# Kernel tuning notes

Hardware: AMD Instinct MI355X
Metric: run time of the kernel (lower is better)

The kernel has to match this reference:

```python
import jax, jax.numpy as jnp
import numpy as np

B, T, E, H, A, NH = 128, 128, 1024, 1024, 64, 8
SCALE = 1.0 / float(np.sqrt(A))


def setup_inputs() -> dict:
    key = jax.random.key(0)
    ks = jax.random.split(key, 10)
    g = lambda k, shape: jax.random.normal(k, shape, dtype=jnp.float32) * 0.02
    return {
        "encs": jax.random.normal(ks[0], (B, E), dtype=jnp.float32),
        "W_ih": g(ks[1], (3 * H, 2 * E)),
        "W_hh": g(ks[2], (3 * H, H)),
        "b_ih": jnp.zeros((3 * H,), jnp.float32),
        "b_hh": jnp.zeros((3 * H,), jnp.float32),
        "W_mu": g(ks[3], (H, E)),
        "b_mu": jnp.zeros((E,), jnp.float32),
        "W_sig": g(ks[4], (H, E)),
        "b_sig": jnp.zeros((E,), jnp.float32),
        "W_q": g(ks[5], (E, NH * A)),
        "b_q": jnp.zeros((NH * A,), jnp.float32),
        "W_k": g(ks[6], (E, NH * A)),
        "b_k": jnp.zeros((NH * A,), jnp.float32),
        "W_v": g(ks[7], (E, NH * A)),
        "b_v": jnp.zeros((NH * A,), jnp.float32),
        "W_o": g(ks[8], (NH * A, E)),
        "b_o": jnp.zeros((E,), jnp.float32),
    }


def reference(encs, W_ih, W_hh, b_ih, b_hh, W_mu, b_mu, W_sig, b_sig,
              W_q, b_q, W_k, b_k, W_v, b_v, W_o, b_o):
    noise_key = jax.random.key(1234)

    def gru(x, h):  # torch.nn.GRUCell math
        gi = x @ W_ih.T + b_ih
        gh = h @ W_hh.T + b_hh
        ir, iz, inn = jnp.split(gi, 3, axis=-1)
        hr, hz, hn = jnp.split(gh, 3, axis=-1)
        r = jax.nn.sigmoid(ir + hr)
        z = jax.nn.sigmoid(iz + hz)
        n = jnp.tanh(inn + r * hn)
        return (1.0 - z) * n + z * h

    def attn_last(s, i):
        # multi_attn(s,s,s)[:, i]: only row i of softmax is needed (rows independent)
        q = (s[:, :, :] @ W_q + b_q)  # (B,T,NH*A)
        q_i = jax.lax.dynamic_index_in_dim(q, i, axis=1, keepdims=False).reshape(B, NH, A)
        k = (s @ W_k + b_k).reshape(B, T, NH, A)
        v = (s @ W_v + b_v).reshape(B, T, NH, A)
        scores = jnp.einsum("bha,bjha->bhj", q_i, k) * SCALE  # (B,NH,T)
        valid = jnp.arange(T) <= i
        scores = jnp.where(valid[None, None, :], scores, -1e30)
        w = jax.nn.softmax(scores, axis=-1)
        ctx = jnp.einsum("bhj,bjha->bha", w, v).reshape(B, NH * A)
        return ctx @ W_o + b_o  # (B,E)

    def step(carry, i):
        h, mus, sigs, context = carry
        x = jnp.concatenate([encs, context], axis=-1)  # (B,2E)
        h = gru(x, h)
        mu = h @ W_mu + b_mu
        sig = jax.nn.softplus(h @ W_sig + b_sig)
        mus = mus.at[:, i].set(mu)
        sigs = sigs.at[:, i].set(sig)
        eps = jax.random.normal(jax.random.fold_in(noise_key, i), (B, T, E), dtype=jnp.float32)
        valid = (jnp.arange(T) <= i)[None, :, None]
        s = jnp.where(valid, mus + eps * sigs, 0.0)
        context = attn_last(s, i)
        return (h, mus, sigs, context), None

    init = (jnp.zeros((B, H), jnp.float32),
            jnp.zeros((B, T, E), jnp.float32),
            jnp.zeros((B, T, E), jnp.float32),
            jnp.zeros((B, E), jnp.float32))
    (h, mus, sigs, _), _ = jax.lax.scan(step, init, jnp.arange(T))
    # final return is s sampled at step T-1 (all positions valid)
    eps_last = jax.random.normal(jax.random.fold_in(noise_key, T - 1), (B, T, E), dtype=jnp.float32)
    return mus + eps_last * sigs
```

## Files before the change

kernel.cpp:

```cpp
#include <hip/hip_runtime.h>

#define B_   128
#define T_   128
#define E_   1024
#define H_   1024
#define A_   64
#define NH_  8
#define G_   3072
#define QK_  512
#define SCALE_ 0.125f

__device__ __forceinline__ unsigned rotl32(unsigned x, int r) {
  return (x << r) | (x >> (32 - r));
}

__device__ __forceinline__ void tf2x32(unsigned k0, unsigned k1,
                                       unsigned x0, unsigned x1,
                                       unsigned& o0, unsigned& o1) {
  unsigned k2 = k0 ^ k1 ^ 0x1BD11BDAu;
  x0 += k0; x1 += k1;
  x0 += x1; x1 = rotl32(x1, 13); x1 ^= x0;
  x0 += x1; x1 = rotl32(x1, 15); x1 ^= x0;
  x0 += x1; x1 = rotl32(x1, 26); x1 ^= x0;
  x0 += x1; x1 = rotl32(x1,  6); x1 ^= x0;
  x0 += k1; x1 += k2 + 1u;
  x0 += x1; x1 = rotl32(x1, 17); x1 ^= x0;
  x0 += x1; x1 = rotl32(x1, 29); x1 ^= x0;
  x0 += x1; x1 = rotl32(x1, 16); x1 ^= x0;
  x0 += x1; x1 = rotl32(x1, 24); x1 ^= x0;
  x0 += k2; x1 += k0 + 2u;
  x0 += x1; x1 = rotl32(x1, 13); x1 ^= x0;
  x0 += x1; x1 = rotl32(x1, 15); x1 ^= x0;
  x0 += x1; x1 = rotl32(x1, 26); x1 ^= x0;
  x0 += x1; x1 = rotl32(x1,  6); x1 ^= x0;
  x0 += k0; x1 += k1 + 3u;
  x0 += x1; x1 = rotl32(x1, 17); x1 ^= x0;
  x0 += x1; x1 = rotl32(x1, 29); x1 ^= x0;
  x0 += x1; x1 = rotl32(x1, 16); x1 ^= x0;
  x0 += x1; x1 = rotl32(x1, 24); x1 ^= x0;
  x0 += k1; x1 += k2 + 4u;
  x0 += x1; x1 = rotl32(x1, 13); x1 ^= x0;
  x0 += x1; x1 = rotl32(x1, 15); x1 ^= x0;
  x0 += x1; x1 = rotl32(x1, 26); x1 ^= x0;
  x0 += x1; x1 = rotl32(x1,  6); x1 ^= x0;
  x0 += k2; x1 += k0 + 5u;
  o0 = x0; o1 = x1;
}

__device__ __forceinline__ float bits_to_normal(unsigned bits) {
  float uf = __uint_as_float((bits >> 9) | 0x3F800000u) - 1.0f;
  const float LO = -0.99999994f;
  float u = fmaxf(LO, uf * 2.0f + LO);
  float w = -log1pf(-u * u);
  float p;
  if (w < 5.0f) {
    w -= 2.5f;
    p = 2.81022636e-08f;
    p = fmaf(p, w, 3.43273939e-07f);
    p = fmaf(p, w, -3.5233877e-06f);
    p = fmaf(p, w, -4.39150654e-06f);
    p = fmaf(p, w, 0.00021858087f);
    p = fmaf(p, w, -0.00125372503f);
    p = fmaf(p, w, -0.00417768164f);
    p = fmaf(p, w, 0.246640727f);
    p = fmaf(p, w, 1.50140941f);
  } else {
    w = sqrtf(w) - 3.0f;
    p = -0.000200214257f;
    p = fmaf(p, w, 0.000100950558f);
    p = fmaf(p, w, 0.00134934322f);
    p = fmaf(p, w, -0.00367342844f);
    p = fmaf(p, w, 0.00573950773f);
    p = fmaf(p, w, -0.0076224613f);
    p = fmaf(p, w, 0.00943887047f);
    p = fmaf(p, w, 1.00167406f);
    p = fmaf(p, w, 2.83297682f);
  }
  return 1.41421356f * p * u;
}

__device__ __forceinline__ float sigmoidf_(float x) {
  return 1.0f / (1.0f + expf(-x));
}

__device__ __forceinline__ float ld_elem(const void* p, long i, int isb) {
  if (isb) {
    unsigned short u = ((const unsigned short*)p)[i];
    return __uint_as_float(((unsigned)u) << 16);
  }
  return ((const float*)p)[i];
}

__global__ __launch_bounds__(256) void sniff_kernel(const void* encs, int* flag) {
  __shared__ int cnt;
  if (threadIdx.x == 0) cnt = 0;
  __syncthreads();
  const unsigned* w = (const unsigned*)encs;
  int c = 0;
  for (int i = threadIdx.x; i < 4096; i += 256) {
    unsigned e7 = (w[i] >> 8) & 0x7F;
    if (e7 >= 0x3B && e7 <= 0x41) c++;
  }
  atomicAdd(&cnt, c);
  __syncthreads();
  if (threadIdx.x == 0) flag[0] = (cnt > 2048) ? 1 : 0;
}

__global__ __launch_bounds__(256) void conv_kernel(const void* src, float* dst,
                                                   long n, const int* flag) {
  long i = (long)blockIdx.x * 256 + threadIdx.x;
  int isb = flag[0];
  if (i < n) dst[i] = ld_elem(src, i, isb);
}

__global__ __launch_bounds__(256) void trans_kernel(
    const void* W_ih, const void* W_hh, const void* W_mu, const void* W_sig,
    const void* W_k, const float* __restrict__ bihF, const float* __restrict__ bhhF,
    float* __restrict__ Wbig, float* __restrict__ Wms, float* __restrict__ WkT,
    float* __restrict__ Wenc4, float* __restrict__ bias4,
    float* __restrict__ xh, float* __restrict__ h, unsigned* __restrict__ skeys,
    const int* flag)
{
  long idx = (long)blockIdx.x * 256 + threadIdx.x;
  int y = blockIdx.y;
  int isb = flag[0];
  if (y == 0) {
    if (idx < 4194304) {
      int e = (int)(idx & 1023); int col = (int)(idx >> 10);
      int j = col >> 2, c = col & 3;
      float v = 0.f;
      if (c < 3) v = ld_elem(W_ih, (long)(c * 1024 + j) * 2048 + 1024 + e, isb);
      Wbig[(long)e * 4096 + col] = v;
    }
  } else if (y == 1) {
    if (idx < 4194304) {
      int e = (int)(idx & 1023); int col = (int)(idx >> 10);
      int j = col >> 2, c = col & 3;
      float v = 0.f;
      if (c == 0)      v = ld_elem(W_hh, (long)j * 1024 + e, isb);
      else if (c == 1) v = ld_elem(W_hh, (long)(1024 + j) * 1024 + e, isb);
      else if (c == 3) v = ld_elem(W_hh, (long)(2048 + j) * 1024 + e, isb);
      Wbig[(long)(1024 + e) * 4096 + col] = v;
    }
  } else if (y == 2) {
    if (idx < 2097152) {
      int k = (int)(idx >> 11), n = (int)(idx & 2047);
      float v = (n < 1024) ? ld_elem(W_mu, (long)k * 1024 + n, isb)
                           : ld_elem(W_sig, (long)k * 1024 + (n - 1024), isb);
      Wms[idx] = v;
    }
  } else if (y == 3) {
    if (idx < 524288) {
      int qk = (int)(idx >> 10), e = (int)(idx & 1023);
      WkT[idx] = ld_elem(W_k, (long)e * 512 + qk, isb);
    }
    if (idx < 4096) {
      int j = (int)(idx >> 2), c = (int)(idx & 3);
      float v;
      if (c == 0)      v = bihF[j] + bhhF[j];
      else if (c == 1) v = bihF[1024 + j] + bhhF[1024 + j];
      else if (c == 2) v = bihF[2048 + j];
      else             v = bhhF[2048 + j];
      bias4[idx] = v;
    }
    if (idx < 262144) xh[idx] = 0.f;
    if (idx < 131072) h[idx] = 0.f;
    if (idx < 128) {
      unsigned o0, o1;
      tf2x32(0u, 1234u, 0u, (unsigned)idx, o0, o1);
      skeys[2 * idx] = o0; skeys[2 * idx + 1] = o1;
    }
  } else {
    if (idx < 4194304) {
      int e = (int)(idx & 1023); int col = (int)(idx >> 10);
      int j = col >> 2, c = col & 3;
      float v = 0.f;
      if (c < 3) v = ld_elem(W_ih, (long)(c * 1024 + j) * 2048 + e, isb);
      Wenc4[(long)e * 4096 + col] = v;
    }
  }
}

__global__ __launch_bounds__(256) void consts_kernel(
    const float* __restrict__ bqF, const float* __restrict__ bkF,
    const float* __restrict__ bvF, const float* __restrict__ boF,
    const float* __restrict__ WkT, const float* __restrict__ WoF,
    float* __restrict__ bqk, float* __restrict__ qbc, float* __restrict__ bvo)
{
  int idx = blockIdx.x * 256 + threadIdx.x;
  int hh = idx >> 10, e = idx & 1023;
  float s = 0.f;
  for (int a = 0; a < 64; ++a)
    s += bqF[hh * 64 + a] * WkT[(long)(hh * 64 + a) * 1024 + e];
  bqk[idx] = s;
  if (idx < 1024) {
    float v = boF[idx];
    for (int ha = 0; ha < 512; ++ha) v += bvF[ha] * WoF[(long)ha * 1024 + idx];
    bvo[idx] = v;
  }
  if (idx < 8) {
    float v = 0.f;
    for (int a = 0; a < 64; ++a) v += bqF[idx * 64 + a] * bkF[idx * 64 + a];
    qbc[idx] = v;
  }
}

__global__ __launch_bounds__(256) void mm128(
    const float* __restrict__ A, long lda, long zA, int nsumA, long psA,
    const float* __restrict__ Bm, long ldb, long zB,
    float* __restrict__ C, long ldc, long zC, long pstride,
    int Ktot, int S)
{
  int zz = blockIdx.z;
  int head = zz / S, sp = zz - head * S;
  int Kc = Ktot / S;
  long kb = (long)sp * Kc;
  A += (long)head * zA;
  Bm += (long)head * zB;
  C += (long)head * zC + (long)sp * pstride;
  long m0 = (long)blockIdx.y * 128;
  long n0 = (long)blockIdx.x * 128;
  __shared__ float As[16][132];
  __shared__ float Bs[16][132];
  int tid = threadIdx.x;
  int tx = tid & 15, ty = tid >> 4;
  int am = tid >> 2, ac = tid & 3;
  int bk = tid >> 5, bn = tid & 31;
  float acc[8][8];
  #pragma unroll
  for (int i = 0; i < 8; ++i)
    #pragma unroll
    for (int j = 0; j < 8; ++j) acc[i][j] = 0.f;

  for (int k0 = 0; k0 < Kc; k0 += 16) {
    const float* Ap0 = A + (m0 + am) * lda + kb + k0 + 4 * ac;
    const float* Ap1 = A + (m0 + am + 64) * lda + kb + k0 + 4 * ac;
    float4 a0 = *(const float4*)Ap0;
    float4 a1 = *(const float4*)Ap1;
    for (int s2 = 1; s2 < nsumA; ++s2) {
      float4 t0 = *(const float4*)(Ap0 + (long)s2 * psA);
      float4 t1 = *(const float4*)(Ap1 + (long)s2 * psA);
      a0.x += t0.x; a0.y += t0.y; a0.z += t0.z; a0.w += t0.w;
      a1.x += t1.x; a1.y += t1.y; a1.z += t1.z; a1.w += t1.w;
    }
    float4 b0 = *(const float4*)(Bm + (kb + k0 + bk) * ldb + n0 + 4 * bn);
    float4 b1 = *(const float4*)(Bm + (kb + k0 + bk + 8) * ldb + n0 + 4 * bn);
    __syncthreads();
    As[4 * ac + 0][am] = a0.x; As[4 * ac + 1][am] = a0.y;
    As[4 * ac + 2][am] = a0.z; As[4 * ac + 3][am] = a0.w;
    As[4 * ac + 0][am + 64] = a1.x; As[4 * ac + 1][am + 64] = a1.y;
    As[4 * ac + 2][am + 64] = a1.z; As[4 * ac + 3][am + 64] = a1.w;
    *(float4*)&Bs[bk][4 * bn] = b0;
    *(float4*)&Bs[bk + 8][4 * bn] = b1;
    __syncthreads();
    #pragma unroll
    for (int kk = 0; kk < 16; ++kk) {
      float4 av0 = *(const float4*)&As[kk][ty * 4];
      float4 av1 = *(const float4*)&As[kk][64 + ty * 4];
      float4 bv0 = *(const float4*)&Bs[kk][tx * 4];
      float4 bv1 = *(const float4*)&Bs[kk][64 + tx * 4];
      float amv[8] = {av0.x, av0.y, av0.z, av0.w, av1.x, av1.y, av1.z, av1.w};
      float bnv[8] = {bv0.x, bv0.y, bv0.z, bv0.w, bv1.x, bv1.y, bv1.z, bv1.w};
      #pragma unroll
      for (int i = 0; i < 8; ++i)
        #pragma unroll
        for (int j = 0; j < 8; ++j)
          acc[i][j] = fmaf(amv[i], bnv[j], acc[i][j]);
    }
  }

  #pragma unroll
  for (int i = 0; i < 8; ++i) {
    long r = m0 + (long)(i >> 2) * 64 + ty * 4 + (i & 3);
    float4 v0 = {acc[i][0], acc[i][1], acc[i][2], acc[i][3]};
    float4 v1 = {acc[i][4], acc[i][5], acc[i][6], acc[i][7]};
    *(float4*)(C + r * ldc + n0 + tx * 4) = v0;
    *(float4*)(C + r * ldc + n0 + 64 + tx * 4) = v1;
  }
}

__global__ __launch_bounds__(256) void mm64s(
    const float* __restrict__ A, long lda, long zA,
    const float* __restrict__ Bm, long ldb, long zB,
    float* __restrict__ C, long ldc, long zC, long pstride,
    int Ktot, int S)
{
  int zz = blockIdx.z;
  int head = zz / S, sp = zz - head * S;
  int Kc = Ktot / S;
  long kb = (long)sp * Kc;
  A += (long)head * zA; Bm += (long)head * zB;
  C += (long)head * zC + (long)sp * pstride;
  long n0 = (long)blockIdx.x * 64;
  long m0 = (long)blockIdx.y * 64;
  __shared__ float As[16][68];
  __shared__ float Bs[16][68];
  int tid = threadIdx.x;
  int tx = tid & 15, ty = tid >> 4;
  int ar = tid >> 2, ac = tid & 3;
  int br = tid >> 4, bc = tid & 15;
  float acc[4][4];
  #pragma unroll
  for (int i = 0; i < 4; ++i)
    #pragma unroll
    for (int j = 0; j < 4; ++j) acc[i][j] = 0.f;

  for (int k0 = 0; k0 < Kc; k0 += 16) {
    float4 a4 = *(const float4*)(A + (m0 + ar) * lda + kb + k0 + 4 * ac);
    float4 b4 = *(const float4*)(Bm + (kb + k0 + br) * ldb + n0 + 4 * bc);
    __syncthreads();
    As[4 * ac + 0][ar] = a4.x; As[4 * ac + 1][ar] = a4.y;
    As[4 * ac + 2][ar] = a4.z; As[4 * ac + 3][ar] = a4.w;
    *(float4*)(&Bs[br][4 * bc]) = b4;
    __syncthreads();
    #pragma unroll
    for (int kk = 0; kk < 16; ++kk) {
      float4 av = *(const float4*)(&As[kk][4 * ty]);
      float4 bv = *(const float4*)(&Bs[kk][4 * tx]);
      float amv[4] = {av.x, av.y, av.z, av.w};
      float bnv[4] = {bv.x, bv.y, bv.z, bv.w};
      #pragma unroll
      for (int im = 0; im < 4; ++im)
        #pragma unroll
        for (int jn = 0; jn < 4; ++jn)
          acc[im][jn] = fmaf(amv[im], bnv[jn], acc[im][jn]);
    }
  }
  #pragma unroll
  for (int im = 0; im < 4; ++im) {
    long m = m0 + ty * 4 + im;
    float4 v = {acc[im][0], acc[im][1], acc[im][2], acc[im][3]};
    *(float4*)(C + m * ldc + n0 + tx * 4) = v;
  }
}

__global__ __launch_bounds__(256) void gru_epi(
    const float* __restrict__ gsumP, const float* __restrict__ gie4,
    const float* __restrict__ bias4, float* __restrict__ h,
    float* __restrict__ xh)
{
  int idx = blockIdx.x * 256 + threadIdx.x;
  int b = idx >> 10, j = idx & 1023;
  float4 v = ((const float4*)gie4)[(long)b * 1024 + j];
  float4 bb = ((const float4*)bias4)[j];
  v.x += bb.x; v.y += bb.y; v.z += bb.z; v.w += bb.w;
  #pragma unroll
  for (int s = 0; s < 8; ++s) {
    float4 t = ((const float4*)gsumP)[(long)s * 131072 + (long)b * 1024 + j];
    v.x += t.x; v.y += t.y; v.z += t.z; v.w += t.w;
  }
  float r = sigmoidf_(v.x);
  float z = sigmoidf_(v.y);
  float n = tanhf(v.z + r * v.w);
  float ho = h[idx];
  float hn = (1.0f - z) * n + z * ho;
  h[idx] = hn;
  xh[(long)b * 2048 + 1024 + j] = hn;
}

__global__ __launch_bounds__(256) void musig_epi(
    const float* __restrict__ msP, const float* __restrict__ bmuF,
    const float* __restrict__ bsigF, float* __restrict__ mus,
    float* __restrict__ sigs, int step)
{
  int idx = blockIdx.x * 256 + threadIdx.x;
  int b = idx >> 11, n = idx & 2047;
  float v = 0.f;
  #pragma unroll
  for (int s = 0; s < 8; ++s) v += msP[(long)s * 262144 + idx];
  if (n < 1024) {
    mus[((long)b * T_ + step) * E_ + n] = v + bmuF[n];
  } else {
    float x = v + bsigF[n - 1024];
    sigs[((long)b * T_ + step) * E_ + (n - 1024)] =
        fmaxf(x, 0.0f) + log1pf(expf(-fabsf(x)));
  }
}

__global__ __launch_bounds__(256) void gen_s(
    const float* __restrict__ mus, const float* __restrict__ sigs,
    float* __restrict__ s, const unsigned* __restrict__ skeys, int step)
{
  int t = blockIdx.x;
  int b = blockIdx.y;
  int e = threadIdx.x * 4;
  unsigned sk0 = skeys[2 * step], sk1 = skeys[2 * step + 1];
  unsigned f = (unsigned)(b * (T_ * E_) + t * E_ + e);
  unsigned o0, o1;
  float nv[4];
  tf2x32(sk0, sk1, 0u, f + 0u, o0, o1); nv[0] = bits_to_normal(o0 ^ o1);
  tf2x32(sk0, sk1, 0u, f + 1u, o0, o1); nv[1] = bits_to_normal(o0 ^ o1);
  tf2x32(sk0, sk1, 0u, f + 2u, o0, o1); nv[2] = bits_to_normal(o0 ^ o1);
  tf2x32(sk0, sk1, 0u, f + 3u, o0, o1); nv[3] = bits_to_normal(o0 ^ o1);
  long i4 = (((long)b * T_ + t) * E_ + e) >> 2;
  float4 mu = ((const float4*)mus)[i4];
  float4 sg = ((const float4*)sigs)[i4];
  float4 out;
  out.x = fmaf(nv[0], sg.x, mu.x);
  out.y = fmaf(nv[1], sg.y, mu.y);
  out.z = fmaf(nv[2], sg.z, mu.z);
  out.w = fmaf(nv[3], sg.w, mu.w);
  ((float4*)s)[i4] = out;
}

__global__ __launch_bounds__(256) void t_kernel(
    const float* __restrict__ qP, const float* __restrict__ WkT,
    const float* __restrict__ bkF, const float* __restrict__ bqk,
    const float* __restrict__ qbc, float* __restrict__ tmat,
    float* __restrict__ qb)
{
  int e = blockIdx.x * 256 + threadIdx.x;
  int hh = blockIdx.y;
  int b0 = blockIdx.z * 8;
  __shared__ float q_l[8][64];
  int tid = threadIdx.x;
  for (int idx2 = tid; idx2 < 512; idx2 += 256) {
    int bb = idx2 >> 6, a = idx2 & 63;
    float v = 0.f;
    #pragma unroll
    for (int s = 0; s < 8; ++s)
      v += qP[(long)s * 65536 + (long)(b0 + bb) * 512 + hh * 64 + a];
    q_l[bb][a] = v;
  }
  __syncthreads();
  float acc[8];
  #pragma unroll
  for (int bb = 0; bb < 8; ++bb) acc[bb] = 0.f;
  for (int a = 0; a < 64; ++a) {
    float wv = WkT[(long)(hh * 64 + a) * 1024 + e];
    #pragma unroll
    for (int bb = 0; bb < 8; ++bb) acc[bb] = fmaf(q_l[bb][a], wv, acc[bb]);
  }
  float bq_ = bqk[hh * 1024 + e];
  #pragma unroll
  for (int bb = 0; bb < 8; ++bb)
    tmat[((long)(b0 + bb) * NH_ + hh) * 1024 + e] = acc[bb] + bq_;
  if (blockIdx.x == 0 && tid < 8) {
    int bb = tid;
    float sm = qbc[hh];
    for (int a = 0; a < 64; ++a) sm += q_l[bb][a] * bkF[hh * 64 + a];
    qb[(b0 + bb) * NH_ + hh] = sm;
  }
}

__global__ __launch_bounds__(256) void scores_kernel(
    const float* __restrict__ s, const float* __restrict__ tmat,
    const float* __restrict__ qb, float* __restrict__ scg, int step)
{
  int b = blockIdx.y;
  int jbase = blockIdx.x * 32;
  __shared__ float s_ch[32][132];
  __shared__ float t_ch[8][132];
  int tid = threadIdx.x;
  int hh = tid >> 5, jj = tid & 31;
  int j = jbase + jj;
  float acc = 0.f;
  for (int e0 = 0; e0 < 1024; e0 += 128) {
    __syncthreads();
    #pragma unroll
    for (int q = 0; q < 4; ++q) {
      int f = tid + q * 256;
      int jr = f >> 5, e4 = f & 31;
      int jg = jbase + jr;
      if (jg <= step)
        *(float4*)&s_ch[jr][e4 * 4] =
            *(const float4*)&s[((long)b * T_ + jg) * E_ + e0 + e4 * 4];
    }
    {
      int e4 = tid & 31, h2 = tid >> 5;
      *(float4*)&t_ch[h2][e4 * 4] =
          *(const float4*)&tmat[((long)b * NH_ + h2) * E_ + e0 + e4 * 4];
    }
    __syncthreads();
    if (j <= step) {
      #pragma unroll
      for (int e4 = 0; e4 < 32; ++e4) {
        float4 sv = *(const float4*)&s_ch[jj][e4 * 4];
        float4 tv = *(const float4*)&t_ch[hh][e4 * 4];
        acc = fmaf(sv.x, tv.x, acc);
        acc = fmaf(sv.y, tv.y, acc);
        acc = fmaf(sv.z, tv.z, acc);
        acc = fmaf(sv.w, tv.w, acc);
      }
    }
  }
  if (j <= step)
    scg[((long)b * NH_ + hh) * T_ + j] = (acc + qb[b * NH_ + hh]) * SCALE_;
}

__global__ __launch_bounds__(256) void ctx_kernel(
    const float* __restrict__ s, const float* __restrict__ scg,
    float* __restrict__ ctxE, int step)
{
  int b = blockIdx.y;
  int et = blockIdx.x;
  __shared__ float w_l[NH_][T_];
  __shared__ float s_l[32][68];
  int tid = threadIdx.x;
  {
    int hh = tid >> 5, l = tid & 31;
    const float* sc = scg + ((long)b * NH_ + hh) * T_;
    float m = -3.0e38f;
    for (int j = l; j <= step; j += 32) m = fmaxf(m, sc[j]);
    for (int off = 16; off; off >>= 1) m = fmaxf(m, __shfl_xor(m, off, 32));
    float d = 0.f;
    for (int j = l; j <= step; j += 32) {
      float pe = expf(sc[j] - m);
      w_l[hh][j] = pe;
      d += pe;
    }
    for (int off = 16; off; off >>= 1) d += __shfl_xor(d, off, 32);
    float inv = 1.0f / d;
    for (int j = l; j <= step; j += 32) w_l[hh][j] *= inv;
  }
  int e = tid & 63, hp = tid >> 6;
  float acc0 = 0.f, acc1 = 0.f;
  for (int jc = 0; jc <= step; jc += 32) {
    __syncthreads();
    #pragma unroll
    for (int q = 0; q < 8; ++q) {
      int f = tid + q * 256;
      int jr = f >> 6, ee = f & 63;
      int jg = jc + jr;
      if (jg <= step)
        s_l[jr][ee] = s[((long)b * T_ + jg) * E_ + et * 64 + ee];
    }
    __syncthreads();
    int jmax = min(31, step - jc);
    for (int jr = 0; jr <= jmax; ++jr) {
      float sv = s_l[jr][e];
      acc0 = fmaf(w_l[hp][jc + jr], sv, acc0);
      acc1 = fmaf(w_l[hp + 4][jc + jr], sv, acc1);
    }
  }
  ctxE[((long)b * NH_ + hp) * E_ + et * 64 + e] = acc0;
  ctxE[((long)b * NH_ + hp + 4) * E_ + et * 64 + e] = acc1;
}

__global__ __launch_bounds__(256) void fin_kernel(
    const float* __restrict__ ctxvP, const float* __restrict__ bvo,
    float* __restrict__ xh)
{
  int i4 = blockIdx.x * 256 + threadIdx.x;
  int b = i4 >> 8, e4 = i4 & 255;
  float4 v = ((const float4*)bvo)[e4];
  #pragma unroll
  for (int s = 0; s < 4; ++s) {
    float4 t = ((const float4*)ctxvP)[(long)s * 32768 + (long)b * 256 + e4];
    v.x += t.x; v.y += t.y; v.z += t.z; v.w += t.w;
  }
  ((float4*)xh)[(long)b * 512 + e4] = v;
}

extern "C" void kernel_launch(void* const* d_in, const int* in_sizes, int n_in,
                              void* d_out, int out_size, void* d_ws, size_t ws_size,
                              hipStream_t stream) {
  (void)in_sizes; (void)n_in; (void)out_size; (void)ws_size;
  const void* encs  = d_in[0];
  const void* W_ih  = d_in[1];
  const void* W_hh  = d_in[2];
  const void* b_ih  = d_in[3];
  const void* b_hh  = d_in[4];
  const void* W_mu  = d_in[5];
  const void* b_mu  = d_in[6];
  const void* W_sig = d_in[7];
  const void* b_sig = d_in[8];
  const void* W_q   = d_in[9];
  const void* b_q   = d_in[10];
  const void* W_k   = d_in[11];
  const void* b_k   = d_in[12];
  const void* W_v   = d_in[13];
  const void* b_v   = d_in[14];
  const void* W_o   = d_in[15];
  const void* b_o   = d_in[16];

  float* s = (float*)d_out;
  float* w = (float*)d_ws;

  int*   flag   = (int*)w;
  float* p      = w + 1024;
  float* WbigF  = p;  p += (size_t)2048 * 4096;
  float* WmsF   = p;  p += (size_t)1024 * 2048;
  float* WkTF   = p;  p += (size_t)512 * 1024;
  float* WqF    = p;  p += (size_t)1024 * 512;
  float* WvF    = p;  p += (size_t)1024 * 512;
  float* WoF    = p;  p += (size_t)512 * 1024;
  float* encsF  = p;  p += (size_t)B_ * E_;
  float* bihF   = p;  p += 4096;
  float* bhhF   = p;  p += 4096;
  float* bmuF   = p;  p += 1024;
  float* bsigF  = p;  p += 1024;
  float* bqF    = p;  p += 1024;
  float* bkF    = p;  p += 1024;
  float* bvF    = p;  p += 1024;
  float* boF    = p;  p += 1024;
  float* bias4  = p;  p += 4096;
  float* bqk    = p;  p += 8192;
  float* qbc    = p;  p += 1024;
  float* bvo    = p;  p += 1024;
  unsigned* skeys = (unsigned*)p; p += 1024;
  float* gie4   = p;  p += (size_t)B_ * 4096;
  float* xh     = p;  p += (size_t)B_ * 2048;
  float* hbuf   = p;  p += (size_t)B_ * 1024;
  float* gsumP  = p;  p += (size_t)8 * B_ * 4096;
  float* musigP = p;  p += (size_t)8 * B_ * 2048;
  float* qP     = p;  p += (size_t)8 * B_ * 512;
  float* tmat   = p;  p += (size_t)B_ * NH_ * E_;
  float* qbv    = p;  p += 1024;
  float* scg    = p;  p += (size_t)B_ * NH_ * T_;
  float* ctxE   = p;  p += (size_t)B_ * NH_ * E_;
  float* ctxhP  = p;  p += (size_t)4 * B_ * 512;
  float* ctxvP  = p;  p += (size_t)4 * B_ * 1024;
  float* mus    = p;  p += (size_t)B_ * T_ * E_;
  float* sigs   = p;  p += (size_t)B_ * T_ * E_;
  float* Wenc4  = gsumP;

  sniff_kernel<<<1, 256, 0, stream>>>(encs, flag);
  auto conv = [&](const void* src, float* dst, long n) {
    conv_kernel<<<dim3((unsigned)((n + 255) / 256)), 256, 0, stream>>>(src, dst, n, flag);
  };
  conv(encs,  encsF, (long)B_ * E_);
  conv(b_ih,  bihF,  G_);
  conv(b_hh,  bhhF,  G_);
  conv(b_mu,  bmuF,  1024);
  conv(b_sig, bsigF, 1024);
  conv(b_q,   bqF,   512);
  conv(b_k,   bkF,   512);
  conv(b_v,   bvF,   512);
  conv(b_o,   boF,   1024);
  conv(W_q,   WqF,   (long)1024 * 512);
  conv(W_v,   WvF,   (long)1024 * 512);
  conv(W_o,   WoF,   (long)512 * 1024);

  trans_kernel<<<dim3(16384, 5), 256, 0, stream>>>(
      W_ih, W_hh, W_mu, W_sig, W_k, bihF, bhhF,
      WbigF, WmsF, WkTF, Wenc4, bias4, xh, hbuf, skeys, flag);
  consts_kernel<<<dim3(32), 256, 0, stream>>>(
      bqF, bkF, bvF, boF, WkTF, WoF, bqk, qbc, bvo);
  mm128<<<dim3(32, 1, 1), 256, 0, stream>>>(
      encsF, 1024, 0, 1, 0, Wenc4, 4096, 0, gie4, 4096, 0, 0, 1024, 1);

  for (int i = 0; i < T_; ++i) {
    mm128<<<dim3(32, 1, 8), 256, 0, stream>>>(
        xh, 2048, 0, 1, 0, WbigF, 4096, 0, gsumP, 4096, 0, 524288, 2048, 8);
    gru_epi<<<dim3(512), 256, 0, stream>>>(gsumP, gie4, bias4, hbuf, xh);
    mm128<<<dim3(16, 1, 8), 256, 0, stream>>>(
        hbuf, 1024, 0, 1, 0, WmsF, 2048, 0, musigP, 2048, 0, 262144, 1024, 8);
    musig_epi<<<dim3(1024), 256, 0, stream>>>(musigP, bmuF, bsigF, mus, sigs, i);
    gen_s<<<dim3(i + 1, B_), 256, 0, stream>>>(mus, sigs, s, skeys, i);
    mm128<<<dim3(4, 1, 8), 256, 0, stream>>>(
        s + (long)i * E_, (long)T_ * E_, 0, 1, 0, WqF, 512, 0,
        qP, 512, 0, 65536, 1024, 8);
    t_kernel<<<dim3(4, 8, 16), 256, 0, stream>>>(
        qP, WkTF, bkF, bqk, qbc, tmat, qbv);
    scores_kernel<<<dim3((i + 32) / 32, B_), 256, 0, stream>>>(
        s, tmat, qbv, scg, i);
    ctx_kernel<<<dim3(16, B_), 256, 0, stream>>>(s, scg, ctxE, i);
    mm64s<<<dim3(1, 2, 32), 256, 0, stream>>>(
        ctxE, 8192, 1024, WvF, 512, 64, ctxhP, 512, 64, 65536, 1024, 4);
    mm128<<<dim3(8, 1, 4), 256, 0, stream>>>(
        ctxhP, 512, 0, 4, 65536, WoF, 1024, 0, ctxvP, 1024, 0, 131072, 512, 4);
    fin_kernel<<<dim3(128), 256, 0, stream>>>(ctxvP, bvo, xh);
  }
}
```

Measured before the change: 27.35 ms.

## Fuse per-step kernel sequence into persistent megakernel with grid barriers

Replaces the 12 kernel launches per time step (about 1500 in total) with one persistent 256-block megakernel. Stages are separated by a software grid barrier built on atomics. The regeneration of earlier s rows is spread over idle blocks and overlapped with the GEMM stages, and the mu/sigma epilogue is fused with sampling of the current row. This removes launch overhead and tail gaps between small kernels. The cost is many grid-wide barriers per step and a co-residency requirement for all 256 blocks, which risks deadlock if they are not all resident.

```diff
diff --git a/kernel.cpp b/kernel.cpp
--- a/kernel.cpp
+++ b/kernel.cpp
@@ -91,9 +91,36 @@
   return ((const float*)p)[i];
 }
 
+#define NBLK_ 256
+
+__device__ __forceinline__ void gsync(unsigned* bar, int tid) {
+  __syncthreads();
+  if (tid == 0) {
+    __threadfence();
+    unsigned g = __hip_atomic_load(&bar[1], __ATOMIC_RELAXED,
+                                   __HIP_MEMORY_SCOPE_AGENT);
+    unsigned a = __hip_atomic_fetch_add(&bar[0], 1u, __ATOMIC_ACQ_REL,
+                                        __HIP_MEMORY_SCOPE_AGENT);
+    if (a == NBLK_ - 1u) {
+      __hip_atomic_store(&bar[0], 0u, __ATOMIC_RELAXED,
+                         __HIP_MEMORY_SCOPE_AGENT);
+      __hip_atomic_store(&bar[1], g + 1u, __ATOMIC_RELEASE,
+                         __HIP_MEMORY_SCOPE_AGENT);
+    } else {
+      while (__hip_atomic_load(&bar[1], __ATOMIC_RELAXED,
+                               __HIP_MEMORY_SCOPE_AGENT) == g) {
+        __builtin_amdgcn_s_sleep(1);
+      }
+      __threadfence();
+    }
+  }
+  __syncthreads();
+}
+
 __global__ __launch_bounds__(256) void sniff_kernel(const void* encs, int* flag) {
   __shared__ int cnt;
   if (threadIdx.x == 0) cnt = 0;
+  if (threadIdx.x < 2) ((unsigned*)flag)[8 + threadIdx.x] = 0u;
   __syncthreads();
   const unsigned* w = (const unsigned*)encs;
   int c = 0;
@@ -205,24 +232,32 @@
   }
 }
 
-__global__ __launch_bounds__(256) void mm128(
-    const float* __restrict__ A, long lda, long zA, int nsumA, long psA,
-    const float* __restrict__ Bm, long ldb, long zB,
-    float* __restrict__ C, long ldc, long zC, long pstride,
-    int Ktot, int S)
+struct MegaArgs {
+  const float *WbigF, *WmsF, *WkTF, *WqF, *WvF, *WoF;
+  const float *bmuF, *bsigF, *bkF, *bias4, *bqk, *qbc, *bvo;
+  const unsigned *skeys;
+  const float *gie4;
+  float *xh, *hbuf, *gsumP, *musigP, *qP, *tmat, *qbv, *scg;
+  float *ctxE, *ctxhP, *ctxvP, *mus, *sigs, *s;
+  unsigned *bar;
+};
+
+__device__ void mm128_dev(float* smem,
+    const float* A, long lda, long zA, int nsumA, long psA,
+    const float* Bm, long ldb, long zB,
+    float* C, long ldc, long zC, long pstride,
+    int Ktot, int S, int bx, int by, int zz, int tid)
 {
-  int zz = blockIdx.z;
   int head = zz / S, sp = zz - head * S;
   int Kc = Ktot / S;
   long kb = (long)sp * Kc;
   A += (long)head * zA;
   Bm += (long)head * zB;
   C += (long)head * zC + (long)sp * pstride;
-  long m0 = (long)blockIdx.y * 128;
-  long n0 = (long)blockIdx.x * 128;
-  __shared__ float As[16][132];
-  __shared__ float Bs[16][132];
-  int tid = threadIdx.x;
+  long m0 = (long)by * 128;
+  long n0 = (long)bx * 128;
+  float* As = smem;
+  float* Bs = smem + 2112;
   int tx = tid & 15, ty = tid >> 4;
   int am = tid >> 2, ac = tid & 3;
   int bk = tid >> 5, bn = tid & 31;
@@ -246,19 +281,19 @@
     float4 b0 = *(const float4*)(Bm + (kb + k0 + bk) * ldb + n0 + 4 * bn);
     float4 b1 = *(const float4*)(Bm + (kb + k0 + bk + 8) * ldb + n0 + 4 * bn);
     __syncthreads();
-    As[4 * ac + 0][am] = a0.x; As[4 * ac + 1][am] = a0.y;
-    As[4 * ac + 2][am] = a0.z; As[4 * ac + 3][am] = a0.w;
-    As[4 * ac + 0][am + 64] = a1.x; As[4 * ac + 1][am + 64] = a1.y;
-    As[4 * ac + 2][am + 64] = a1.z; As[4 * ac + 3][am + 64] = a1.w;
-    *(float4*)&Bs[bk][4 * bn] = b0;
-    *(float4*)&Bs[bk + 8][4 * bn] = b1;
+    As[(4 * ac + 0) * 132 + am] = a0.x; As[(4 * ac + 1) * 132 + am] = a0.y;
+    As[(4 * ac + 2) * 132 + am] = a0.z; As[(4 * ac + 3) * 132 + am] = a0.w;
+    As[(4 * ac + 0) * 132 + am + 64] = a1.x; As[(4 * ac + 1) * 132 + am + 64] = a1.y;
+    As[(4 * ac + 2) * 132 + am + 64] = a1.z; As[(4 * ac + 3) * 132 + am + 64] = a1.w;
+    *(float4*)&Bs[bk * 132 + 4 * bn] = b0;
+    *(float4*)&Bs[(bk + 8) * 132 + 4 * bn] = b1;
     __syncthreads();
     #pragma unroll
     for (int kk = 0; kk < 16; ++kk) {
-      float4 av0 = *(const float4*)&As[kk][ty * 4];
-      float4 av1 = *(const float4*)&As[kk][64 + ty * 4];
-      float4 bv0 = *(const float4*)&Bs[kk][tx * 4];
-      float4 bv1 = *(const float4*)&Bs[kk][64 + tx * 4];
+      float4 av0 = *(const float4*)&As[kk * 132 + ty * 4];
+      float4 av1 = *(const float4*)&As[kk * 132 + 64 + ty * 4];
+      float4 bv0 = *(const float4*)&Bs[kk * 132 + tx * 4];
+      float4 bv1 = *(const float4*)&Bs[kk * 132 + 64 + tx * 4];
       float amv[8] = {av0.x, av0.y, av0.z, av0.w, av1.x, av1.y, av1.z, av1.w};
       float bnv[8] = {bv0.x, bv0.y, bv0.z, bv0.w, bv1.x, bv1.y, bv1.z, bv1.w};
       #pragma unroll
@@ -279,23 +314,21 @@
   }
 }
 
-__global__ __launch_bounds__(256) void mm64s(
-    const float* __restrict__ A, long lda, long zA,
-    const float* __restrict__ Bm, long ldb, long zB,
-    float* __restrict__ C, long ldc, long zC, long pstride,
-    int Ktot, int S)
+__device__ void mm64s_dev(float* smem,
+    const float* A, long lda, long zA, int nsumA, long psA,
+    const float* Bm, long ldb, long zB,
+    float* C, long ldc, long zC, long pstride,
+    int Ktot, int S, int bx, int by, int zz, int tid)
 {
-  int zz = blockIdx.z;
   int head = zz / S, sp = zz - head * S;
   int Kc = Ktot / S;
   long kb = (long)sp * Kc;
   A += (long)head * zA; Bm += (long)head * zB;
   C += (long)head * zC + (long)sp * pstride;
-  long n0 = (long)blockIdx.x * 64;
-  long m0 = (long)blockIdx.y * 64;
-  __shared__ float As[16][68];
-  __shared__ float Bs[16][68];
-  int tid = threadIdx.x;
+  long n0 = (long)bx * 64;
+  long m0 = (long)by * 64;
+  float* As = smem;
+  float* Bs = smem + 1088;
   int tx = tid & 15, ty = tid >> 4;
   int ar = tid >> 2, ac = tid & 3;
   int br = tid >> 4, bc = tid & 15;
@@ -306,17 +339,22 @@
     for (int j = 0; j < 4; ++j) acc[i][j] = 0.f;
 
   for (int k0 = 0; k0 < Kc; k0 += 16) {
-    float4 a4 = *(const float4*)(A + (m0 + ar) * lda + kb + k0 + 4 * ac);
+    const float* Ap = A + (m0 + ar) * lda + kb + k0 + 4 * ac;
+    float4 a4 = *(const float4*)Ap;
+    for (int s2 = 1; s2 < nsumA; ++s2) {
+      float4 t = *(const float4*)(Ap + (long)s2 * psA);
+      a4.x += t.x; a4.y += t.y; a4.z += t.z; a4.w += t.w;
+    }
     float4 b4 = *(const float4*)(Bm + (kb + k0 + br) * ldb + n0 + 4 * bc);
     __syncthreads();
-    As[4 * ac + 0][ar] = a4.x; As[4 * ac + 1][ar] = a4.y;
-    As[4 * ac + 2][ar] = a4.z; As[4 * ac + 3][ar] = a4.w;
-    *(float4*)(&Bs[br][4 * bc]) = b4;
+    As[(4 * ac + 0) * 68 + ar] = a4.x; As[(4 * ac + 1) * 68 + ar] = a4.y;
+    As[(4 * ac + 2) * 68 + ar] = a4.z; As[(4 * ac + 3) * 68 + ar] = a4.w;
+    *(float4*)(&Bs[br * 68 + 4 * bc]) = b4;
     __syncthreads();
     #pragma unroll
     for (int kk = 0; kk < 16; ++kk) {
-      float4 av = *(const float4*)(&As[kk][4 * ty]);
-      float4 bv = *(const float4*)(&Bs[kk][4 * tx]);
+      float4 av = *(const float4*)(&As[kk * 68 + 4 * ty]);
+      float4 bv = *(const float4*)(&Bs[kk * 68 + 4 * tx]);
       float amv[4] = {av.x, av.y, av.z, av.w};
       float bnv[4] = {bv.x, bv.y, bv.z, bv.w};
       #pragma unroll
@@ -334,124 +372,115 @@
   }
 }
 
-__global__ __launch_bounds__(256) void gru_epi(
-    const float* __restrict__ gsumP, const float* __restrict__ gie4,
-    const float* __restrict__ bias4, float* __restrict__ h,
-    float* __restrict__ xh)
-{
-  int idx = blockIdx.x * 256 + threadIdx.x;
+__device__ void gru_dev(int idx, const MegaArgs& a) {
   int b = idx >> 10, j = idx & 1023;
-  float4 v = ((const float4*)gie4)[(long)b * 1024 + j];
-  float4 bb = ((const float4*)bias4)[j];
-  v.x += bb.x; v.y += bb.y; v.z += bb.z; v.w += bb.w;
-  #pragma unroll
-  for (int s = 0; s < 8; ++s) {
-    float4 t = ((const float4*)gsumP)[(long)s * 131072 + (long)b * 1024 + j];
+  float4 v = ((const float4*)a.gie4)[(long)b * 1024 + j];
+  float4 bb4 = ((const float4*)a.bias4)[j];
+  v.x += bb4.x; v.y += bb4.y; v.z += bb4.z; v.w += bb4.w;
+  #pragma unroll
+  for (int s2 = 0; s2 < 8; ++s2) {
+    float4 t = ((const float4*)a.gsumP)[(long)s2 * 131072 + (long)b * 1024 + j];
     v.x += t.x; v.y += t.y; v.z += t.z; v.w += t.w;
   }
   float r = sigmoidf_(v.x);
   float z = sigmoidf_(v.y);
   float n = tanhf(v.z + r * v.w);
-  float ho = h[idx];
+  float ho = a.hbuf[idx];
   float hn = (1.0f - z) * n + z * ho;
-  h[idx] = hn;
-  xh[(long)b * 2048 + 1024 + j] = hn;
-}
-
-__global__ __launch_bounds__(256) void musig_epi(
-    const float* __restrict__ msP, const float* __restrict__ bmuF,
-    const float* __restrict__ bsigF, float* __restrict__ mus,
-    float* __restrict__ sigs, int step)
-{
-  int idx = blockIdx.x * 256 + threadIdx.x;
-  int b = idx >> 11, n = idx & 2047;
-  float v = 0.f;
-  #pragma unroll
-  for (int s = 0; s < 8; ++s) v += msP[(long)s * 262144 + idx];
-  if (n < 1024) {
-    mus[((long)b * T_ + step) * E_ + n] = v + bmuF[n];
-  } else {
-    float x = v + bsigF[n - 1024];
-    sigs[((long)b * T_ + step) * E_ + (n - 1024)] =
-        fmaxf(x, 0.0f) + log1pf(expf(-fabsf(x)));
-  }
-}
-
-__global__ __launch_bounds__(256) void gen_s(
-    const float* __restrict__ mus, const float* __restrict__ sigs,
-    float* __restrict__ s, const unsigned* __restrict__ skeys, int step)
-{
-  int t = blockIdx.x;
-  int b = blockIdx.y;
-  int e = threadIdx.x * 4;
-  unsigned sk0 = skeys[2 * step], sk1 = skeys[2 * step + 1];
-  unsigned f = (unsigned)(b * (T_ * E_) + t * E_ + e);
-  unsigned o0, o1;
-  float nv[4];
-  tf2x32(sk0, sk1, 0u, f + 0u, o0, o1); nv[0] = bits_to_normal(o0 ^ o1);
-  tf2x32(sk0, sk1, 0u, f + 1u, o0, o1); nv[1] = bits_to_normal(o0 ^ o1);
-  tf2x32(sk0, sk1, 0u, f + 2u, o0, o1); nv[2] = bits_to_normal(o0 ^ o1);
-  tf2x32(sk0, sk1, 0u, f + 3u, o0, o1); nv[3] = bits_to_normal(o0 ^ o1);
-  long i4 = (((long)b * T_ + t) * E_ + e) >> 2;
-  float4 mu = ((const float4*)mus)[i4];
-  float4 sg = ((const float4*)sigs)[i4];
-  float4 out;
-  out.x = fmaf(nv[0], sg.x, mu.x);
-  out.y = fmaf(nv[1], sg.y, mu.y);
-  out.z = fmaf(nv[2], sg.z, mu.z);
-  out.w = fmaf(nv[3], sg.w, mu.w);
-  ((float4*)s)[i4] = out;
-}
-
-__global__ __launch_bounds__(256) void t_kernel(
-    const float* __restrict__ qP, const float* __restrict__ WkT,
-    const float* __restrict__ bkF, const float* __restrict__ bqk,
-    const float* __restrict__ qbc, float* __restrict__ tmat,
-    float* __restrict__ qb)
-{
-  int e = blockIdx.x * 256 + threadIdx.x;
-  int hh = blockIdx.y;
-  int b0 = blockIdx.z * 8;
-  __shared__ float q_l[8][64];
-  int tid = threadIdx.x;
+  a.hbuf[idx] = hn;
+  a.xh[(long)b * 2048 + 1024 + j] = hn;
+}
+
+__device__ void musig_gen_dev(int bid, int tid, int step, const MegaArgs& a) {
+  unsigned sk0 = a.skeys[2 * step], sk1 = a.skeys[2 * step + 1];
+  #pragma unroll
+  for (int k = 0; k < 2; ++k) {
+    int el = bid * 256 + tid + k * 65536;
+    int b = el >> 10, e = el & 1023;
+    float mu = a.bmuF[e], xg = a.bsigF[e];
+    #pragma unroll
+    for (int s2 = 0; s2 < 8; ++s2) {
+      mu += a.musigP[(long)s2 * 262144 + (long)b * 2048 + e];
+      xg += a.musigP[(long)s2 * 262144 + (long)b * 2048 + 1024 + e];
+    }
+    float sig = fmaxf(xg, 0.0f) + log1pf(expf(-fabsf(xg)));
+    a.mus[((long)b * T_ + step) * E_ + e] = mu;
+    a.sigs[((long)b * T_ + step) * E_ + e] = sig;
+    unsigned f = (unsigned)(b * (T_ * E_) + step * E_ + e);
+    unsigned o0, o1;
+    tf2x32(sk0, sk1, 0u, f, o0, o1);
+    a.s[((long)b * T_ + step) * E_ + e] = fmaf(bits_to_normal(o0 ^ o1), sig, mu);
+  }
+}
+
+__device__ void gen_rows_dev(int lo, int hi, int lbid, int nb, int step,
+                             const MegaArgs& a, int tid) {
+  int nvb = (hi - lo) * 128;
+  if (nvb <= 0) return;
+  unsigned sk0 = a.skeys[2 * step], sk1 = a.skeys[2 * step + 1];
+  for (int vb = lbid; vb < nvb; vb += nb) {
+    int t = lo + (vb >> 7);
+    int b = vb & 127;
+    int e = tid * 4;
+    unsigned f = (unsigned)(b * (T_ * E_) + t * E_ + e);
+    unsigned o0, o1;
+    float nv[4];
+    tf2x32(sk0, sk1, 0u, f + 0u, o0, o1); nv[0] = bits_to_normal(o0 ^ o1);
+    tf2x32(sk0, sk1, 0u, f + 1u, o0, o1); nv[1] = bits_to_normal(o0 ^ o1);
+    tf2x32(sk0, sk1, 0u, f + 2u, o0, o1); nv[2] = bits_to_normal(o0 ^ o1);
+    tf2x32(sk0, sk1, 0u, f + 3u, o0, o1); nv[3] = bits_to_normal(o0 ^ o1);
+    long i4 = (((long)b * T_ + t) * E_ + e) >> 2;
+    float4 mu = ((const float4*)a.mus)[i4];
+    float4 sg = ((const float4*)a.sigs)[i4];
+    float4 out;
+    out.x = fmaf(nv[0], sg.x, mu.x);
+    out.y = fmaf(nv[1], sg.y, mu.y);
+    out.z = fmaf(nv[2], sg.z, mu.z);
+    out.w = fmaf(nv[3], sg.w, mu.w);
+    ((float4*)a.s)[i4] = out;
+  }
+}
+
+__device__ void tk_dev(float* smem, int vb, const MegaArgs& a, int tid) {
+  int bx = vb & 3, hh = (vb >> 2) & 7, bz = vb >> 5;
+  int e = bx * 256 + tid;
+  int b0 = bz * 8;
+  float* q_l = smem;
+  __syncthreads();
   for (int idx2 = tid; idx2 < 512; idx2 += 256) {
-    int bb = idx2 >> 6, a = idx2 & 63;
+    int bb = idx2 >> 6, aa = idx2 & 63;
     float v = 0.f;
     #pragma unroll
-    for (int s = 0; s < 8; ++s)
-      v += qP[(long)s * 65536 + (long)(b0 + bb) * 512 + hh * 64 + a];
-    q_l[bb][a] = v;
+    for (int s2 = 0; s2 < 8; ++s2)
+      v += a.qP[(long)s2 * 65536 + (long)(b0 + bb) * 512 + hh * 64 + aa];
+    q_l[bb * 64 + aa] = v;
   }
   __syncthreads();
   float acc[8];
   #pragma unroll
   for (int bb = 0; bb < 8; ++bb) acc[bb] = 0.f;
-  for (int a = 0; a < 64; ++a) {
-    float wv = WkT[(long)(hh * 64 + a) * 1024 + e];
-    #pragma unroll
-    for (int bb = 0; bb < 8; ++bb) acc[bb] = fmaf(q_l[bb][a], wv, acc[bb]);
-  }
-  float bq_ = bqk[hh * 1024 + e];
+  for (int aa = 0; aa < 64; ++aa) {
+    float wv = a.WkTF[(long)(hh * 64 + aa) * 1024 + e];
+    #pragma unroll
+    for (int bb = 0; bb < 8; ++bb) acc[bb] = fmaf(q_l[bb * 64 + aa], wv, acc[bb]);
+  }
+  float bq_ = a.bqk[hh * 1024 + e];
   #pragma unroll
   for (int bb = 0; bb < 8; ++bb)
-    tmat[((long)(b0 + bb) * NH_ + hh) * 1024 + e] = acc[bb] + bq_;
-  if (blockIdx.x == 0 && tid < 8) {
+    a.tmat[((long)(b0 + bb) * NH_ + hh) * 1024 + e] = acc[bb] + bq_;
+  if (bx == 0 && tid < 8) {
     int bb = tid;
-    float sm = qbc[hh];
-    for (int a = 0; a < 64; ++a) sm += q_l[bb][a] * bkF[hh * 64 + a];
-    qb[(b0 + bb) * NH_ + hh] = sm;
-  }
-}
-
-__global__ __launch_bounds__(256) void scores_kernel(
-    const float* __restrict__ s, const float* __restrict__ tmat,
-    const float* __restrict__ qb, float* __restrict__ scg, int step)
-{
-  int b = blockIdx.y;
-  int jbase = blockIdx.x * 32;
-  __shared__ float s_ch[32][132];
-  __shared__ float t_ch[8][132];
-  int tid = threadIdx.x;
+    float sm2 = a.qbc[hh];
+    for (int aa = 0; aa < 64; ++aa) sm2 += q_l[bb * 64 + aa] * a.bkF[hh * 64 + aa];
+    a.qbv[(b0 + bb) * NH_ + hh] = sm2;
+  }
+}
+
+__device__ void sc_dev(float* smem, int jt, int b, int step, const MegaArgs& a,
+                       int tid) {
+  int jbase = jt * 32;
+  float* s_ch = smem;
+  float* t_ch = smem + 32 * 132;
   int hh = tid >> 5, jj = tid & 31;
   int j = jbase + jj;
   float acc = 0.f;
@@ -463,20 +492,20 @@
       int jr = f >> 5, e4 = f & 31;
       int jg = jbase + jr;
       if (jg <= step)
-        *(float4*)&s_ch[jr][e4 * 4] =
-            *(const float4*)&s[((long)b * T_ + jg) * E_ + e0 + e4 * 4];
+        *(float4*)&s_ch[jr * 132 + e4 * 4] =
+            *(const float4*)&a.s[((long)b * T_ + jg) * E_ + e0 + e4 * 4];
     }
     {
       int e4 = tid & 31, h2 = tid >> 5;
-      *(float4*)&t_ch[h2][e4 * 4] =
-          *(const float4*)&tmat[((long)b * NH_ + h2) * E_ + e0 + e4 * 4];
+      *(float4*)&t_ch[h2 * 132 + e4 * 4] =
+          *(const float4*)&a.tmat[((long)b * NH_ + h2) * E_ + e0 + e4 * 4];
     }
     __syncthreads();
     if (j <= step) {
       #pragma unroll
       for (int e4 = 0; e4 < 32; ++e4) {
-        float4 sv = *(const float4*)&s_ch[jj][e4 * 4];
-        float4 tv = *(const float4*)&t_ch[hh][e4 * 4];
+        float4 sv = *(const float4*)&s_ch[jj * 132 + e4 * 4];
+        float4 tv = *(const float4*)&t_ch[hh * 132 + e4 * 4];
         acc = fmaf(sv.x, tv.x, acc);
         acc = fmaf(sv.y, tv.y, acc);
         acc = fmaf(sv.z, tv.z, acc);
@@ -485,33 +514,29 @@
     }
   }
   if (j <= step)
-    scg[((long)b * NH_ + hh) * T_ + j] = (acc + qb[b * NH_ + hh]) * SCALE_;
-}
-
-__global__ __launch_bounds__(256) void ctx_kernel(
-    const float* __restrict__ s, const float* __restrict__ scg,
-    float* __restrict__ ctxE, int step)
-{
-  int b = blockIdx.y;
-  int et = blockIdx.x;
-  __shared__ float w_l[NH_][T_];
-  __shared__ float s_l[32][68];
-  int tid = threadIdx.x;
+    a.scg[((long)b * NH_ + hh) * T_ + j] = (acc + a.qbv[b * NH_ + hh]) * SCALE_;
+}
+
+__device__ void ctx_dev(float* smem, int et, int b, int step, const MegaArgs& a,
+                        int tid) {
+  float* w_l = smem;
+  float* s_l = smem + 1024;
+  __syncthreads();
   {
     int hh = tid >> 5, l = tid & 31;
-    const float* sc = scg + ((long)b * NH_ + hh) * T_;
+    const float* sc = a.scg + ((long)b * NH_ + hh) * T_;
     float m = -3.0e38f;
     for (int j = l; j <= step; j += 32) m = fmaxf(m, sc[j]);
     for (int off = 16; off; off >>= 1) m = fmaxf(m, __shfl_xor(m, off, 32));
     float d = 0.f;
     for (int j = l; j <= step; j += 32) {
       float pe = expf(sc[j] - m);
-      w_l[hh][j] = pe;
+      w_l[hh * T_ + j] = pe;
       d += pe;
     }
     for (int off = 16; off; off >>= 1) d += __shfl_xor(d, off, 32);
     float inv = 1.0f / d;
-    for (int j = l; j <= step; j += 32) w_l[hh][j] *= inv;
+    for (int j = l; j <= step; j += 32) w_l[hh * T_ + j] *= inv;
   }
   int e = tid & 63, hp = tid >> 6;
   float acc0 = 0.f, acc1 = 0.f;
@@ -523,33 +548,96 @@
       int jr = f >> 6, ee = f & 63;
       int jg = jc + jr;
       if (jg <= step)
-        s_l[jr][ee] = s[((long)b * T_ + jg) * E_ + et * 64 + ee];
+        s_l[jr * 68 + ee] = a.s[((long)b * T_ + jg) * E_ + et * 64 + ee];
     }
     __syncthreads();
     int jmax = min(31, step - jc);
     for (int jr = 0; jr <= jmax; ++jr) {
-      float sv = s_l[jr][e];
-      acc0 = fmaf(w_l[hp][jc + jr], sv, acc0);
-      acc1 = fmaf(w_l[hp + 4][jc + jr], sv, acc1);
-    }
-  }
-  ctxE[((long)b * NH_ + hp) * E_ + et * 64 + e] = acc0;
-  ctxE[((long)b * NH_ + hp + 4) * E_ + et * 64 + e] = acc1;
-}
-
-__global__ __launch_bounds__(256) void fin_kernel(
-    const float* __restrict__ ctxvP, const float* __restrict__ bvo,
-    float* __restrict__ xh)
+      float sv = s_l[jr * 68 + e];
+      acc0 = fmaf(w_l[hp * T_ + jc + jr], sv, acc0);
+      acc1 = fmaf(w_l[(hp + 4) * T_ + jc + jr], sv, acc1);
+    }
+  }
+  a.ctxE[((long)b * NH_ + hp) * E_ + et * 64 + e] = acc0;
+  a.ctxE[((long)b * NH_ + hp + 4) * E_ + et * 64 + e] = acc1;
+}
+
+__device__ void fin_dev(int vb, int tid, const MegaArgs& a) {
+  int i4 = vb * 256 + tid;
+  int b = i4 >> 8, e4 = i4 & 255;
+  float4 v = ((const float4*)a.bvo)[e4];
+  #pragma unroll
+  for (int s2 = 0; s2 < 8; ++s2) {
+    float4 t = ((const float4*)a.ctxvP)[(long)s2 * 32768 + (long)b * 256 + e4];
+    v.x += t.x; v.y += t.y; v.z += t.z; v.w += t.w;
+  }
+  ((float4*)a.xh)[(long)b * 512 + e4] = v;
+}
+
+__global__ __launch_bounds__(256) void mm128_k(
+    const float* A, long lda, long zA, int nsumA, long psA,
+    const float* Bm, long ldb, long zB,
+    float* C, long ldc, long zC, long pstride, int Ktot, int S)
 {
-  int i4 = blockIdx.x * 256 + threadIdx.x;
-  int b = i4 >> 8, e4 = i4 & 255;
-  float4 v = ((const float4*)bvo)[e4];
-  #pragma unroll
-  for (int s = 0; s < 4; ++s) {
-    float4 t = ((const float4*)ctxvP)[(long)s * 32768 + (long)b * 256 + e4];
-    v.x += t.x; v.y += t.y; v.z += t.z; v.w += t.w;
-  }
-  ((float4*)xh)[(long)b * 512 + e4] = v;
+  __shared__ __align__(16) float smem[4224];
+  mm128_dev(smem, A, lda, zA, nsumA, psA, Bm, ldb, zB, C, ldc, zC, pstride,
+            Ktot, S, blockIdx.x, blockIdx.y, blockIdx.z, threadIdx.x);
+}
+
+__global__ __launch_bounds__(256) void megakernel(MegaArgs a) {
+  const int bid = blockIdx.x;
+  const int tid = threadIdx.x;
+  unsigned* bar = a.bar;
+  __shared__ __align__(16) float smem[5280];
+
+  #pragma unroll 1
+  for (int i = 0; i < T_; ++i) {
+    int r1 = (i * 7) / 12;
+    int r2 = (i * 10) / 12;
+    mm128_dev(smem, a.xh, 2048, 0, 1, 0, a.WbigF, 4096, 0,
+              a.gsumP, 4096, 0, 524288, 2048, 8, bid & 31, 0, bid >> 5, tid);
+    gen_rows_dev(0, r1, bid, 256, i, a, tid);
+    gsync(bar, tid);
+    gru_dev(bid * 256 + tid, a);
+    gru_dev((bid + 256) * 256 + tid, a);
+    gsync(bar, tid);
+    if (bid < 128)
+      mm128_dev(smem, a.hbuf, 1024, 0, 1, 0, a.WmsF, 2048, 0,
+                a.musigP, 2048, 0, 262144, 1024, 8, bid & 15, 0, bid >> 4, tid);
+    else
+      gen_rows_dev(r1, r2, bid - 128, 128, i, a, tid);
+    gsync(bar, tid);
+    musig_gen_dev(bid, tid, i, a);
+    gsync(bar, tid);
+    if (bid < 128)
+      mm64s_dev(smem, a.s + (long)i * E_, (long)T_ * E_, 0, 1, 0,
+                a.WqF, 512, 0, a.qP, 512, 0, 65536, 1024, 8,
+                bid & 7, (bid >> 3) & 1, bid >> 4, tid);
+    else
+      gen_rows_dev(r2, i, bid - 128, 128, i, a, tid);
+    gsync(bar, tid);
+    for (int vb = bid; vb < 512; vb += 256) tk_dev(smem, vb, a, tid);
+    gsync(bar, tid);
+    {
+      int nvb = ((i + 32) / 32) * 128;
+      for (int vb = bid; vb < nvb; vb += 256)
+        sc_dev(smem, vb >> 7, vb & 127, i, a, tid);
+    }
+    gsync(bar, tid);
+    for (int vb = bid; vb < 2048; vb += 256)
+      ctx_dev(smem, vb & 15, vb >> 4, i, a, tid);
+    gsync(bar, tid);
+    if (bid < 64)
+      mm64s_dev(smem, a.ctxE, 8192, 1024, 1, 0, a.WvF, 512, 64,
+                a.ctxhP, 512, 64, 65536, 1024, 4, 0, bid & 1, bid >> 1, tid);
+    gsync(bar, tid);
+    mm64s_dev(smem, a.ctxhP, 512, 0, 4, 65536, a.WoF, 1024, 0,
+              a.ctxvP, 1024, 0, 131072, 512, 8,
+              bid & 15, (bid >> 4) & 1, bid >> 5, tid);
+    gsync(bar, tid);
+    if (bid < 128) fin_dev(bid, tid, a);
+    gsync(bar, tid);
+  }
 }
 
 extern "C" void kernel_launch(void* const* d_in, const int* in_sizes, int n_in,
@@ -578,6 +666,7 @@
   float* w = (float*)d_ws;
 
   int*   flag   = (int*)w;
+  unsigned* bar = ((unsigned*)w) + 8;
   float* p      = w + 1024;
   float* WbigF  = p;  p += (size_t)2048 * 4096;
   float* WmsF   = p;  p += (size_t)1024 * 2048;
@@ -610,10 +699,10 @@
   float* scg    = p;  p += (size_t)B_ * NH_ * T_;
   float* ctxE   = p;  p += (size_t)B_ * NH_ * E_;
   float* ctxhP  = p;  p += (size_t)4 * B_ * 512;
-  float* ctxvP  = p;  p += (size_t)4 * B_ * 1024;
   float* mus    = p;  p += (size_t)B_ * T_ * E_;
   float* sigs   = p;  p += (size_t)B_ * T_ * E_;
   float* Wenc4  = gsumP;
+  float* ctxvP  = gsumP;
 
   sniff_kernel<<<1, 256, 0, stream>>>(encs, flag);
   auto conv = [&](const void* src, float* dst, long n) {
@@ -637,29 +726,19 @@
       WbigF, WmsF, WkTF, Wenc4, bias4, xh, hbuf, skeys, flag);
   consts_kernel<<<dim3(32), 256, 0, stream>>>(
       bqF, bkF, bvF, boF, WkTF, WoF, bqk, qbc, bvo);
-  mm128<<<dim3(32, 1, 1), 256, 0, stream>>>(
+  mm128_k<<<dim3(32, 1, 1), 256, 0, stream>>>(
       encsF, 1024, 0, 1, 0, Wenc4, 4096, 0, gie4, 4096, 0, 0, 1024, 1);
 
-  for (int i = 0; i < T_; ++i) {
-    mm128<<<dim3(32, 1, 8), 256, 0, stream>>>(
-        xh, 2048, 0, 1, 0, WbigF, 4096, 0, gsumP, 4096, 0, 524288, 2048, 8);
-    gru_epi<<<dim3(512), 256, 0, stream>>>(gsumP, gie4, bias4, hbuf, xh);
-    mm128<<<dim3(16, 1, 8), 256, 0, stream>>>(
-        hbuf, 1024, 0, 1, 0, WmsF, 2048, 0, musigP, 2048, 0, 262144, 1024, 8);
-    musig_epi<<<dim3(1024), 256, 0, stream>>>(musigP, bmuF, bsigF, mus, sigs, i);
-    gen_s<<<dim3(i + 1, B_), 256, 0, stream>>>(mus, sigs, s, skeys, i);
-    mm128<<<dim3(4, 1, 8), 256, 0, stream>>>(
-        s + (long)i * E_, (long)T_ * E_, 0, 1, 0, WqF, 512, 0,
-        qP, 512, 0, 65536, 1024, 8);
-    t_kernel<<<dim3(4, 8, 16), 256, 0, stream>>>(
-        qP, WkTF, bkF, bqk, qbc, tmat, qbv);
-    scores_kernel<<<dim3((i + 32) / 32, B_), 256, 0, stream>>>(
-        s, tmat, qbv, scg, i);
-    ctx_kernel<<<dim3(16, B_), 256, 0, stream>>>(s, scg, ctxE, i);
-    mm64s<<<dim3(1, 2, 32), 256, 0, stream>>>(
-        ctxE, 8192, 1024, WvF, 512, 64, ctxhP, 512, 64, 65536, 1024, 4);
-    mm128<<<dim3(8, 1, 4), 256, 0, stream>>>(
-        ctxhP, 512, 0, 4, 65536, WoF, 1024, 0, ctxvP, 1024, 0, 131072, 512, 4);
-    fin_kernel<<<dim3(128), 256, 0, stream>>>(ctxvP, bvo, xh);
-  }
-}
+  MegaArgs ma;
+  ma.WbigF = WbigF; ma.WmsF = WmsF; ma.WkTF = WkTF;
+  ma.WqF = WqF; ma.WvF = WvF; ma.WoF = WoF;
+  ma.bmuF = bmuF; ma.bsigF = bsigF; ma.bkF = bkF;
+  ma.bias4 = bias4; ma.bqk = bqk; ma.qbc = qbc; ma.bvo = bvo;
+  ma.skeys = skeys; ma.gie4 = gie4;
+  ma.xh = xh; ma.hbuf = hbuf; ma.gsumP = gsumP; ma.musigP = musigP;
+  ma.qP = qP; ma.tmat = tmat; ma.qbv = qbv; ma.scg = scg;
+  ma.ctxE = ctxE; ma.ctxhP = ctxhP; ma.ctxvP = ctxvP;
+  ma.mus = mus; ma.sigs = sigs; ma.s = s;
+  ma.bar = bar;
+  megakernel<<<dim3(256), dim3(256), 0, stream>>>(ma);
+}
```

Measured after the change: 87.33 ms. +219.3%, slower.
